# Kernel optimization log

Hardware: AMD Instinct MI355X
Metric: run time of the kernel (lower is better)

## Reference

```python
import jax, jax.numpy as jnp
import numpy as np

# Model constants (match init_kwargs)
NUM_HEADS = 8
IN_BITS = 64
N_STATE = 256
N_OUT = 64
K_CONN = 8            # n_bits_per_output_neuron
HASH = 65536          # hash_size
K_BITS = 3            # routing key bits
B = 128               # batch of independent sequences
T = 128               # timesteps (windows) per sequence


def setup_inputs() -> dict:
    key = jax.random.key(0)
    k1, k2, k3, k4, k5, k6 = jax.random.split(key, 6)
    # flat bit sequences, split into T windows of IN_BITS in reference()
    bits = jax.random.randint(k1, (B, T * IN_BITS), 0, 2, dtype=jnp.int32)
    # state layer: full connectivity (default n_bits_per_state_neuron =
    # input_bits + n_state_neurons), hashed addressing via random odd-ish
    # integer coefficients dotted with the bit vector, mod HASH.
    total_in = IN_BITS + N_STATE  # 320
    state_coeffs = jax.random.randint(k2, (N_STATE, total_in), 1, HASH, dtype=jnp.int32)
    state_mem = jax.random.uniform(k3, (N_STATE, HASH), dtype=jnp.float32)
    # output heads: each neuron connects to K_CONN random state bits
    head_conn = jax.random.randint(k4, (NUM_HEADS, N_OUT, K_CONN), 0, N_STATE, dtype=jnp.int32)
    head_coeffs = jax.random.randint(k5, (NUM_HEADS, N_OUT, K_CONN), 1, HASH, dtype=jnp.int32)
    head_mem = jax.random.uniform(k6, (NUM_HEADS, N_OUT, HASH), dtype=jnp.float32)
    return {
        "bits": bits,
        "state_coeffs": state_coeffs,
        "state_mem": state_mem,
        "head_conn": head_conn,
        "head_coeffs": head_coeffs,
        "head_mem": head_mem,
    }


def reference(bits, state_coeffs, state_mem, head_conn, head_coeffs, head_mem):
    # windows: [B, T, IN_BITS]
    windows = bits.reshape(B, T, IN_BITS)
    n_state, hash_size = state_mem.shape

    def step(state, w):  # state: [B, N_STATE] int32 bits; w: [B, IN_BITS]
        x = jnp.concatenate([w, state], axis=1)                 # [B, IN+N]
        addr = (x @ state_coeffs.T) % hash_size                 # hashed address [B, N]
        vals = state_mem[jnp.arange(n_state), addr]             # gather [B, N]
        new_state = (vals >= 0.5).astype(jnp.int32)             # RAM output bits
        return new_state, None

    state0 = jnp.zeros((B, n_state), jnp.int32)
    final_state, _ = jax.lax.scan(step, state0, jnp.swapaxes(windows, 0, 1))

    # all output heads read the shared final state
    sel = final_state[:, head_conn]                             # [B, H, O, K]
    addr_h = jnp.einsum('bhok,hok->bho', sel, head_coeffs) % hash_size
    head_vals = head_mem[jnp.arange(NUM_HEADS)[:, None],
                         jnp.arange(N_OUT)[None, :], addr_h]    # [B, H, O]

    # kv routing: pack last K_BITS bits of the final window (MSB first)
    last_w = windows[:, -1, :]
    pow2 = 2 ** jnp.arange(K_BITS - 1, -1, -1)
    head_idx = jnp.sum(last_w[:, -K_BITS:] * pow2, axis=1) % NUM_HEADS  # [B]

    out = head_vals[jnp.arange(B), head_idx]                    # [B, N_OUT]
    return out
```

## Files before the change

### kernel.cpp

```cpp
#include <hip/hip_runtime.h>
#include <stdint.h>

#define T_ 128

typedef int v4i __attribute__((ext_vector_type(4)));

__global__ void prep_bfrag(const int* __restrict__ sc, uint4* __restrict__ bf) {
  int gid = blockIdx.x * 256 + threadIdx.x;
  if (gid >= 160 * 64) return;
  int mf = gid >> 6, l = gid & 63;
  int tau = mf / 10, rem = mf % 10;
  int kap = rem >> 1, h = rem & 1;
  int j = 16 * tau + (l & 15);
  int kinb = (l >> 4) * 16;
  unsigned wout[4];
#pragma unroll
  for (int r = 0; r < 4; ++r) {
    unsigned wrd = 0;
#pragma unroll
    for (int be = 0; be < 4; ++be) {
      int kin = kinb + 4 * r + be;
      int col = (kap == 0) ? kin : 64 + ((kap - 1) << 6) + kin;
      unsigned c = (unsigned)sc[j * 320 + col];
      unsigned byte = (h ? (c >> 8) : c) & 0xFFu;
      byte = (byte - 128u) & 0xFFu;
      wrd |= byte << (8 * be);
    }
    wout[r] = wrd;
  }
  bf[gid] = make_uint4(wout[0], wout[1], wout[2], wout[3]);
}

__global__ void prep_wbits(const int* __restrict__ bits,
                           unsigned long long* __restrict__ wb) {
  int gid = blockIdx.x * 256 + threadIdx.x;
  int wv = gid >> 6, lane = gid & 63;
  unsigned long long m = __ballot(bits[gid] != 0);
  if (lane == 0) wb[wv] = m;
}

__global__ void prep_bitpack(const float* __restrict__ sm,
                             unsigned long long* __restrict__ packed) {
  int base = blockIdx.x * (256 * 32) + threadIdx.x;
  int lane = threadIdx.x & 63;
#pragma unroll 1
  for (int it = 0; it < 32; ++it) {
    int idx = base + it * 256;
    float v = sm[idx];
    unsigned long long m = __ballot(v >= 0.5f);
    if (lane == 0) packed[idx >> 6] = m;
  }
}

static __device__ __forceinline__ v4i expand16(unsigned b16) {
  v4i a;
#pragma unroll
  for (int r = 0; r < 4; ++r) {
    unsigned nib = (b16 >> (4 * r)) & 0xFu;
    a[r] = (int)((nib * 0x00204081u) & 0x01010101u);
  }
  return a;
}

__global__ __launch_bounds__(512) void scan_heads(
    const uint4* __restrict__ bfrag,
    const unsigned long long* __restrict__ wbits,
    const unsigned* __restrict__ packed32,
    const int* __restrict__ head_conn,
    const int* __restrict__ head_coeffs,
    const float* __restrict__ head_mem,
    float* __restrict__ out) {
  __shared__ __align__(16) unsigned msh[2][8];
  const int tid = threadIdx.x;
  const int b = blockIdx.x;
  const int w = tid >> 6, l = tid & 63;
  const int qq = (l >> 4) & 3;
  const int sh = 16 * (qq & 1);
  const int wi = qq >> 1;

  v4i bf[2][5][2];
#pragma unroll
  for (int i = 0; i < 2; ++i)
#pragma unroll
    for (int k = 0; k < 5; ++k)
#pragma unroll
      for (int h = 0; h < 2; ++h) {
        int mf = ((2 * w + i) * 5 + k) * 2 + h;
        bf[i][k][h] = __builtin_bit_cast(v4i, bfrag[mf * 64 + l]);
      }

  unsigned words[8];
#pragma unroll
  for (int i = 0; i < 8; ++i) words[i] = 0u;
  unsigned long long wcur = wbits[b * 128];

  v4i acc[2][2];
  {
    v4i aw = expand16((unsigned)((wcur >> (16 * qq)) & 0xFFFFu));
    v4i z = (v4i){0, 0, 0, 0};
#pragma unroll
    for (int i = 0; i < 2; ++i)
#pragma unroll
      for (int h = 0; h < 2; ++h)
        acc[i][h] = __builtin_amdgcn_mfma_i32_16x16x64_i8(aw, bf[i][0][h], z, 0, 0, 0);
  }

#pragma unroll 1
  for (int t = 0; t < T_; ++t) {
    unsigned NB = (unsigned)__popcll(wcur);
#pragma unroll
    for (int i = 0; i < 8; ++i) NB += (unsigned)__popc(words[i]);

#pragma unroll
    for (int c = 0; c < 4; ++c) {
      v4i a = expand16((words[2 * c + wi] >> sh) & 0xFFFFu);
      acc[0][0] = __builtin_amdgcn_mfma_i32_16x16x64_i8(a, bf[0][c + 1][0], acc[0][0], 0, 0, 0);
      acc[0][1] = __builtin_amdgcn_mfma_i32_16x16x64_i8(a, bf[0][c + 1][1], acc[0][1], 0, 0, 0);
      acc[1][0] = __builtin_amdgcn_mfma_i32_16x16x64_i8(a, bf[1][c + 1][0], acc[1][0], 0, 0, 0);
      acc[1][1] = __builtin_amdgcn_mfma_i32_16x16x64_i8(a, bf[1][c + 1][1], acc[1][1], 0, 0, 0);
    }

    int tn = (t + 1 < T_) ? t + 1 : t;
    unsigned long long wnext = wbits[b * 128 + tn];

    unsigned corr = (NB * 32896u) & 0xFFFFu;
    unsigned lo = (unsigned)((l & 16) ? acc[1][0][0] : acc[0][0][0]);
    unsigned hi = (unsigned)((l & 16) ? acc[1][1][0] : acc[0][1][0]);
    unsigned ad = (lo + (hi << 8) + corr) & 0xFFFFu;

    unsigned bitv = 0;
    if (l < 32) {
      unsigned word = packed32[((size_t)(32 * w + l) << 11) + (ad >> 5)];
      bitv = (word >> (ad & 31)) & 1u;
    }
    unsigned long long mq = __ballot(bitv != 0u);
    if (l == 0) msh[t & 1][w] = (unsigned)mq;

    {
      v4i aw = expand16((unsigned)((wnext >> (16 * qq)) & 0xFFFFu));
      v4i z = (v4i){0, 0, 0, 0};
#pragma unroll
      for (int i = 0; i < 2; ++i)
#pragma unroll
        for (int h = 0; h < 2; ++h)
          acc[i][h] = __builtin_amdgcn_mfma_i32_16x16x64_i8(aw, bf[i][0][h], z, 0, 0, 0);
    }

    __syncthreads();

    uint4 u0 = *((const uint4*)&msh[t & 1][0]);
    uint4 u1 = *((const uint4*)&msh[t & 1][4]);
    words[0] = u0.x; words[1] = u0.y; words[2] = u0.z; words[3] = u0.w;
    words[4] = u1.x; words[5] = u1.y; words[6] = u1.z; words[7] = u1.w;
    wcur = wnext;
  }

  if (w == 0) {
    int h = (int)((((wcur >> 61) & 1) << 2) | (((wcur >> 62) & 1) << 1) |
                  ((wcur >> 63) & 1));
    int ho = h * 64 + l;
    const int4* cn4 = (const int4*)(head_conn + ho * 8);
    const int4* cf4 = (const int4*)(head_coeffs + ho * 8);
    int4 cna = cn4[0], cnb = cn4[1];
    int4 cfa = cf4[0], cfb = cf4[1];
    int cns[8] = {cna.x, cna.y, cna.z, cna.w, cnb.x, cnb.y, cnb.z, cnb.w};
    int cfs[8] = {cfa.x, cfa.y, cfa.z, cfa.w, cfb.x, cfb.y, cfb.z, cfb.w};
    unsigned addr = 0;
#pragma unroll
    for (int k = 0; k < 8; ++k) {
      unsigned bit = (words[cns[k] >> 5] >> (cns[k] & 31)) & 1u;
      addr += bit * (unsigned)cfs[k];
    }
    addr &= 0xFFFFu;
    out[b * 64 + l] = head_mem[((size_t)ho << 16) + addr];
  }
}

extern "C" void kernel_launch(void* const* d_in, const int* in_sizes, int n_in,
                              void* d_out, int out_size, void* d_ws, size_t ws_size,
                              hipStream_t stream) {
  const int*   bits         = (const int*)d_in[0];
  const int*   state_coeffs = (const int*)d_in[1];
  const float* state_mem    = (const float*)d_in[2];
  const int*   head_conn    = (const int*)d_in[3];
  const int*   head_coeffs  = (const int*)d_in[4];
  const float* head_mem     = (const float*)d_in[5];
  float* out = (float*)d_out;

  char* ws = (char*)d_ws;
  uint4*              bfrag  = (uint4*)ws;
  unsigned long long* wbits  = (unsigned long long*)(ws + (160 << 10));
  unsigned*           packed = (unsigned*)(ws + (288 << 10));

  prep_bfrag<<<40, 256, 0, stream>>>(state_coeffs, bfrag);
  prep_wbits<<<4096, 256, 0, stream>>>(bits, wbits);
  prep_bitpack<<<2048, 256, 0, stream>>>(state_mem, (unsigned long long*)packed);
  scan_heads<<<128, 512, 0, stream>>>(bfrag, wbits, packed,
                                      head_conn, head_coeffs, head_mem, out);
}
```

Measured before the change: 348.9 us.

## Halve scan block to 4 waves, keep state as byte array in LDS

The recurrent scan block shrinks from 8 to 4 waves, with each wave owning 64 state neurons through 8 MFMA accumulators instead of 4. The state is stored as an int8 byte array in shared memory, so the next step's A fragments come from direct LDS vector loads rather than bit-expansion from packed words. Popcounts are precomputed per wave. All 64 lanes now do the gather, the wnext load is issued earlier, and the next window's MFMA is overlapped with the gather latency. The aim is to cut per-step barrier cost across waves and shorten the serial dependency chain, at the cost of more MFMAs per wave and higher register pressure.

```diff
diff --git a/kernel.cpp b/kernel.cpp
--- a/kernel.cpp
+++ b/kernel.cpp
@@ -62,7 +62,7 @@
   return a;
 }
 
-__global__ __launch_bounds__(512) void scan_heads(
+__global__ __launch_bounds__(256, 1) void scan_heads(
     const uint4* __restrict__ bfrag,
     const unsigned long long* __restrict__ wbits,
     const unsigned* __restrict__ packed32,
@@ -70,88 +70,94 @@
     const int* __restrict__ head_coeffs,
     const float* __restrict__ head_mem,
     float* __restrict__ out) {
-  __shared__ __align__(16) unsigned msh[2][8];
+  __shared__ __align__(16) unsigned char ab[2][256];
+  __shared__ __align__(16) unsigned mcnt[2][4];
   const int tid = threadIdx.x;
   const int b = blockIdx.x;
   const int w = tid >> 6, l = tid & 63;
-  const int qq = (l >> 4) & 3;
-  const int sh = 16 * (qq & 1);
-  const int wi = qq >> 1;
-
-  v4i bf[2][5][2];
-#pragma unroll
-  for (int i = 0; i < 2; ++i)
+  const int qq = l >> 4;
+  const int j = 64 * w + l;
+
+  v4i bf[4][5][2];
+#pragma unroll
+  for (int i = 0; i < 4; ++i)
 #pragma unroll
     for (int k = 0; k < 5; ++k)
 #pragma unroll
       for (int h = 0; h < 2; ++h) {
-        int mf = ((2 * w + i) * 5 + k) * 2 + h;
+        int mf = ((4 * w + i) * 5 + k) * 2 + h;
         bf[i][k][h] = __builtin_bit_cast(v4i, bfrag[mf * 64 + l]);
       }
 
-  unsigned words[8];
-#pragma unroll
-  for (int i = 0; i < 8; ++i) words[i] = 0u;
+  ab[0][tid] = (unsigned char)0;
+  if (tid < 4) mcnt[0][tid] = 0u;
+
   unsigned long long wcur = wbits[b * 128];
-
-  v4i acc[2][2];
+  const unsigned* pkrow = packed32 + ((size_t)j << 11);
+
+  v4i acc[4][2];
   {
     v4i aw = expand16((unsigned)((wcur >> (16 * qq)) & 0xFFFFu));
     v4i z = (v4i){0, 0, 0, 0};
 #pragma unroll
-    for (int i = 0; i < 2; ++i)
+    for (int i = 0; i < 4; ++i)
 #pragma unroll
       for (int h = 0; h < 2; ++h)
         acc[i][h] = __builtin_amdgcn_mfma_i32_16x16x64_i8(aw, bf[i][0][h], z, 0, 0, 0);
   }
-
+  __syncthreads();
+
+  int cur = 0;
 #pragma unroll 1
   for (int t = 0; t < T_; ++t) {
-    unsigned NB = (unsigned)__popcll(wcur);
-#pragma unroll
-    for (int i = 0; i < 8; ++i) NB += (unsigned)__popc(words[i]);
+    int tn = (t + 1 < T_) ? t + 1 : t;
+    unsigned long long wnext = wbits[b * 128 + tn];
+
+    uint4 cz = *((const uint4*)&mcnt[cur][0]);
+    unsigned NB = cz.x + cz.y + cz.z + cz.w + (unsigned)__popcll(wcur);
 
 #pragma unroll
     for (int c = 0; c < 4; ++c) {
-      v4i a = expand16((words[2 * c + wi] >> sh) & 0xFFFFu);
+      v4i a = *((const v4i*)&ab[cur][64 * c + 16 * qq]);
       acc[0][0] = __builtin_amdgcn_mfma_i32_16x16x64_i8(a, bf[0][c + 1][0], acc[0][0], 0, 0, 0);
       acc[0][1] = __builtin_amdgcn_mfma_i32_16x16x64_i8(a, bf[0][c + 1][1], acc[0][1], 0, 0, 0);
       acc[1][0] = __builtin_amdgcn_mfma_i32_16x16x64_i8(a, bf[1][c + 1][0], acc[1][0], 0, 0, 0);
       acc[1][1] = __builtin_amdgcn_mfma_i32_16x16x64_i8(a, bf[1][c + 1][1], acc[1][1], 0, 0, 0);
-    }
-
-    int tn = (t + 1 < T_) ? t + 1 : t;
-    unsigned long long wnext = wbits[b * 128 + tn];
+      acc[2][0] = __builtin_amdgcn_mfma_i32_16x16x64_i8(a, bf[2][c + 1][0], acc[2][0], 0, 0, 0);
+      acc[2][1] = __builtin_amdgcn_mfma_i32_16x16x64_i8(a, bf[2][c + 1][1], acc[2][1], 0, 0, 0);
+      acc[3][0] = __builtin_amdgcn_mfma_i32_16x16x64_i8(a, bf[3][c + 1][0], acc[3][0], 0, 0, 0);
+      acc[3][1] = __builtin_amdgcn_mfma_i32_16x16x64_i8(a, bf[3][c + 1][1], acc[3][1], 0, 0, 0);
+    }
 
     unsigned corr = (NB * 32896u) & 0xFFFFu;
-    unsigned lo = (unsigned)((l & 16) ? acc[1][0][0] : acc[0][0][0]);
-    unsigned hi = (unsigned)((l & 16) ? acc[1][1][0] : acc[0][1][0]);
+    unsigned lo01 = (l & 16) ? (unsigned)acc[1][0][0] : (unsigned)acc[0][0][0];
+    unsigned lo23 = (l & 16) ? (unsigned)acc[3][0][0] : (unsigned)acc[2][0][0];
+    unsigned hi01 = (l & 16) ? (unsigned)acc[1][1][0] : (unsigned)acc[0][1][0];
+    unsigned hi23 = (l & 16) ? (unsigned)acc[3][1][0] : (unsigned)acc[2][1][0];
+    unsigned lo = (l & 32) ? lo23 : lo01;
+    unsigned hi = (l & 32) ? hi23 : hi01;
     unsigned ad = (lo + (hi << 8) + corr) & 0xFFFFu;
 
-    unsigned bitv = 0;
-    if (l < 32) {
-      unsigned word = packed32[((size_t)(32 * w + l) << 11) + (ad >> 5)];
-      bitv = (word >> (ad & 31)) & 1u;
-    }
-    unsigned long long mq = __ballot(bitv != 0u);
-    if (l == 0) msh[t & 1][w] = (unsigned)mq;
+    unsigned word = pkrow[ad >> 5];
 
     {
       v4i aw = expand16((unsigned)((wnext >> (16 * qq)) & 0xFFFFu));
       v4i z = (v4i){0, 0, 0, 0};
 #pragma unroll
-      for (int i = 0; i < 2; ++i)
+      for (int i = 0; i < 4; ++i)
 #pragma unroll
         for (int h = 0; h < 2; ++h)
           acc[i][h] = __builtin_amdgcn_mfma_i32_16x16x64_i8(aw, bf[i][0][h], z, 0, 0, 0);
     }
 
+    unsigned bitv = (word >> (ad & 31)) & 1u;
+    unsigned long long mq = __ballot(bitv != 0u);
+    int nxt = cur ^ 1;
+    ab[nxt][j] = (unsigned char)bitv;
+    if (l == 0) mcnt[nxt][w] = (unsigned)__popcll(mq);
+
     __syncthreads();
-
-    uint4 u0 = *((const uint4*)&msh[t & 1][0]);
-    uint4 u1 = *((const uint4*)&msh[t & 1][4]);
-    words[0] = u0.x; words[1] = u0.y; words[2] = u0.z; words[3] = u0.w;
-    words[4] = u1.x; words[5] = u1.y; words[6] = u1.z; words[7] = u1.w;
+    cur = nxt;
     wcur = wnext;
   }
 
@@ -168,8 +174,7 @@
     unsigned addr = 0;
 #pragma unroll
     for (int k = 0; k < 8; ++k) {
-      unsigned bit = (words[cns[k] >> 5] >> (cns[k] & 31)) & 1u;
-      addr += bit * (unsigned)cfs[k];
+      addr += (unsigned)ab[cur][cns[k]] * (unsigned)cfs[k];
     }
     addr &= 0xFFFFu;
     out[b * 64 + l] = head_mem[((size_t)ho << 16) + addr];
@@ -195,6 +200,6 @@
   prep_bfrag<<<40, 256, 0, stream>>>(state_coeffs, bfrag);
   prep_wbits<<<4096, 256, 0, stream>>>(bits, wbits);
   prep_bitpack<<<2048, 256, 0, stream>>>(state_mem, (unsigned long long*)packed);
-  scan_heads<<<128, 512, 0, stream>>>(bfrag, wbits, packed,
+  scan_heads<<<128, 256, 0, stream>>>(bfrag, wbits, packed,
                                       head_conn, head_coeffs, head_mem, out);
 }
```

Result: faster. 324.1 us (-7.1%).
